# Kernel tuning notes

Measured on AMD Instinct MI355X. Metric: run time of the kernel, lower is better.

## Reference

```python
import jax, jax.numpy as jnp
import numpy as np

BIG = 1e11  # torch code replaces zero counts with 1e11 before dividing
N_LABELS = 5


def _label_mean(state, func):
    """Masked mean per label (1..5). state [..., S, H], func [..., S] int.
    Returns aug [..., 5, H], aug_mask [..., 5] bool. Zero-count labels -> 0
    (sum is exactly 0 and denom is BIG, matching the torch zero-init path)."""
    mask = (func[..., None] == jnp.arange(1, N_LABELS + 1)).astype(state.dtype)  # [...,S,5]
    sums = jnp.einsum('...sl,...sh->...lh', mask, state)                          # [...,5,H]
    counts = mask.sum(axis=-2)                                                    # [...,5]
    aug_mask = counts > 0
    denom = jnp.where(aug_mask, counts, jnp.asarray(BIG, state.dtype))
    return sums / denom[..., None], aug_mask


def _masked_mean(state, func):
    """Mean over all non-pad (func != 0) sentences. state [..., S, H]."""
    m = (func != 0).astype(state.dtype)
    s = jnp.einsum('...s,...sh->...h', m, state)
    c = m.sum(axis=-1)
    pm = c > 0
    denom = jnp.where(pm, c, jnp.asarray(BIG, state.dtype))
    return s / denom[..., None], pm


def setup_inputs() -> dict:
    key = jax.random.key(0)
    k1, k2, k3, k4 = jax.random.split(key, 4)
    B, TS, H = 8, 512, 512       # batch, tar_n_sents, enc_hidden_size
    D, RS = 32, 256              # ref_n_docs, ref_n_sents
    return {
        'tarsent_state': jax.random.normal(k1, (B, TS, H), jnp.float32),
        'tar_func': jax.random.randint(k2, (B, TS), 0, 6),
        'refsent_state': jax.random.normal(k3, (B, D, RS, H), jnp.float32),
        'ref_func': jax.random.randint(k4, (B, D, RS), 0, 6),
    }


def reference(tarsent_state, tar_func, refsent_state, ref_func):
    # tar_aug_state [B,5,H], tar_aug_mask [B,5]
    tar_aug, tar_aug_mask = _label_mean(tarsent_state, tar_func)
    # ref_aug_state [B,D,5,H], ref_aug_mask [B,D,5]
    ref_aug, ref_aug_mask = _label_mean(refsent_state, ref_func)
    # tarpaper_state [B,H], refpaper_state [B,D,H]
    tarpaper_state, tar_mask2 = _masked_mean(tarsent_state, tar_func)
    refpaper_state, ref_mask2 = _masked_mean(refsent_state, ref_func)
    return (tar_aug, tar_aug_mask, ref_aug, ref_aug_mask,
            tarpaper_state, tar_mask2, refpaper_state, ref_mask2)
```

## Files before the change

### kernel.cpp

```cpp
#include <hip/hip_runtime.h>


#define H      512
#define HV     128
#define NL     5
#define BIGF   1e11f
#define CHUNK  64
#define NITER  (CHUNK / 2)
#define BATCH  8

#define OFF_TAR_AUG       0
#define OFF_TAR_AUG_MASK  20480
#define OFF_REF_AUG       20520
#define OFF_REF_AUG_MASK  675880
#define OFF_TARPAPER      677160
#define OFF_TAR_MASK2     681256
#define OFF_REFPAPER      681264
#define OFF_REF_MASK2     812336

#define NCHUNK_REF 4
#define NCHUNK_TAR 8
#define NBLK_REF   1024
#define NBLK1      1088
#define WSUM_ELEMS ((size_t)NBLK1 * NL * H)
#define WCNT_OFF_B (WSUM_ELEMS * 4)
#define WS_NEED    (WCNT_OFF_B + (size_t)NBLK1 * NL * 4)

__device__ inline float4 f4add(float4 a, float4 b) {
    a.x += b.x; a.y += b.y; a.z += b.z; a.w += b.w; return a;
}
__device__ inline float4 f4scale(float4 a, float s) {
    a.x *= s; a.y *= s; a.z *= s; a.w *= s; return a;
}
__device__ inline float4 f4fma(float w, float4 v, float4 a) {
    a.x = fmaf(w, v.x, a.x); a.y = fmaf(w, v.y, a.y);
    a.z = fmaf(w, v.z, a.z); a.w = fmaf(w, v.w, a.w); return a;
}

__global__ __launch_bounds__(256) void emenc_stage1(
    const float* __restrict__ tar_state, const int* __restrict__ tar_func,
    const float* __restrict__ ref_state, const int* __restrict__ ref_func,
    float* __restrict__ wsum, int* __restrict__ wcnt)
{
    __shared__ int    sfunc[CHUNK];
    __shared__ float4 spart[HV * NL];

    const int b = blockIdx.x;
    const float* state;
    const int*   func;
    int s0;
    if (b < NBLK_REF) {
        const int seg = b >> 2, ch = b & 3;
        state = ref_state + (size_t)seg * 256 * H;
        func  = ref_func  + seg * 256;
        s0    = ch * CHUNK;
    } else {
        const int q = b - NBLK_REF;
        const int seg = q >> 3, ch = q & 7;
        state = tar_state + (size_t)seg * 512 * H;
        func  = tar_func  + seg * 512;
        s0    = ch * CHUNK;
    }

    const int tid = threadIdx.x;
    if (tid < CHUNK) sfunc[tid] = func[s0 + tid];
    __syncthreads();

    const int col   = tid & (HV - 1);
    const int phase = tid >> 7;

    float4 a1 = {0,0,0,0}, a2 = {0,0,0,0}, a3 = {0,0,0,0},
           a4 = {0,0,0,0}, a5 = {0,0,0,0};

    const float4* colp = ((const float4*)(state + (size_t)s0 * H)) + col
                         + (size_t)phase * HV;

    #pragma unroll
    for (int batch = 0; batch < NITER / BATCH; ++batch) {
        const int j0 = batch * BATCH;
        float4 v[BATCH];
        int    lb[BATCH];
        #pragma unroll
        for (int k = 0; k < BATCH; ++k)
            v[k] = colp[(size_t)(2 * (j0 + k)) * HV];
        #pragma unroll
        for (int k = 0; k < BATCH; ++k)
            lb[k] = sfunc[2 * (j0 + k) + phase];
        #pragma unroll
        for (int k = 0; k < BATCH; ++k) {
            const int l = lb[k];
            const float w1 = (l == 1) ? 1.0f : 0.0f;
            const float w2 = (l == 2) ? 1.0f : 0.0f;
            const float w3 = (l == 3) ? 1.0f : 0.0f;
            const float w4 = (l == 4) ? 1.0f : 0.0f;
            const float w5 = (l == 5) ? 1.0f : 0.0f;
            a1 = f4fma(w1, v[k], a1);
            a2 = f4fma(w2, v[k], a2);
            a3 = f4fma(w3, v[k], a3);
            a4 = f4fma(w4, v[k], a4);
            a5 = f4fma(w5, v[k], a5);
        }
    }

    if (phase == 1) {
        spart[col * NL + 0] = a1;
        spart[col * NL + 1] = a2;
        spart[col * NL + 2] = a3;
        spart[col * NL + 3] = a4;
        spart[col * NL + 4] = a5;
    }
    __syncthreads();

    if (phase == 0) {
        a1 = f4add(a1, spart[col * NL + 0]);
        a2 = f4add(a2, spart[col * NL + 1]);
        a3 = f4add(a3, spart[col * NL + 2]);
        a4 = f4add(a4, spart[col * NL + 3]);
        a5 = f4add(a5, spart[col * NL + 4]);

        float* wb = wsum + (size_t)b * NL * H;
        ((float4*)(wb + 0 * H))[col] = a1;
        ((float4*)(wb + 1 * H))[col] = a2;
        ((float4*)(wb + 2 * H))[col] = a3;
        ((float4*)(wb + 3 * H))[col] = a4;
        ((float4*)(wb + 4 * H))[col] = a5;
    }

    if (tid < NL) {
        int c = 0;
        #pragma unroll
        for (int i = 0; i < CHUNK; ++i) c += (sfunc[i] == tid + 1) ? 1 : 0;
        wcnt[b * NL + tid] = c;
    }
}

__global__ __launch_bounds__(128) void emenc_stage2(
    const float* __restrict__ wsum, const int* __restrict__ wcnt,
    float* __restrict__ out)
{
    const int bb   = blockIdx.x;
    const int seg  = bb / 6;
    const int role = bb - seg * 6;

    int nch, wb0;
    float *aug, *augmask, *paper, *mask2;
    if (seg < 256) {
        nch = NCHUNK_REF; wb0 = seg * NCHUNK_REF;
        aug     = out + OFF_REF_AUG      + (size_t)seg * NL * H;
        augmask = out + OFF_REF_AUG_MASK + seg * NL;
        paper   = out + OFF_REFPAPER     + (size_t)seg * H;
        mask2   = out + OFF_REF_MASK2    + seg;
    } else {
        const int q = seg - 256;
        nch = NCHUNK_TAR; wb0 = NBLK_REF + q * NCHUNK_TAR;
        aug     = out + OFF_TAR_AUG      + (size_t)q * NL * H;
        augmask = out + OFF_TAR_AUG_MASK + q * NL;
        paper   = out + OFF_TARPAPER     + (size_t)q * H;
        mask2   = out + OFF_TAR_MASK2    + q;
    }

    const int col = threadIdx.x;

    if (role < NL) {
        int c = 0;
        for (int ch = 0; ch < nch; ch++) c += wcnt[(wb0 + ch) * NL + role];
        float4 s = {0,0,0,0};
        for (int ch = 0; ch < nch; ch++)
            s = f4add(s, ((const float4*)(wsum + (size_t)(wb0 + ch) * NL * H
                                          + (size_t)role * H))[col]);
        const float inv = 1.0f / (c > 0 ? (float)c : BIGF);
        ((float4*)(aug + (size_t)role * H))[col] = f4scale(s, inv);
        if (col == 0) augmask[role] = c > 0 ? 1.0f : 0.0f;
    } else {
        int ct = 0;
        for (int ch = 0; ch < nch; ch++) {
            #pragma unroll
            for (int l = 0; l < NL; l++) ct += wcnt[(wb0 + ch) * NL + l];
        }
        float4 t = {0,0,0,0};
        for (int ch = 0; ch < nch; ch++) {
            const float4* wb = (const float4*)(wsum + (size_t)(wb0 + ch) * NL * H);
            #pragma unroll
            for (int l = 0; l < NL; l++) t = f4add(t, wb[l * HV + col]);
        }
        ((float4*)paper)[col] = f4scale(t, 1.0f / (ct > 0 ? (float)ct : BIGF));
        if (col == 0) mask2[0] = ct > 0 ? 1.0f : 0.0f;
    }
}

__global__ __launch_bounds__(256) void emenc_single(
    const float* __restrict__ tar_state, const int* __restrict__ tar_func,
    const float* __restrict__ ref_state, const int* __restrict__ ref_func,
    float* __restrict__ out)
{
    __shared__ int    sfunc[512];
    __shared__ float4 spart[HV * NL];
    __shared__ int    scnt[NL];

    const int b = blockIdx.x;
    const float* state;
    const int*   func;
    int S;
    float *aug, *augmask, *paper, *mask2;

    if (b < 256) {
        state   = ref_state + (size_t)b * 256 * H;
        func    = ref_func  + b * 256;
        S       = 256;
        aug     = out + OFF_REF_AUG      + (size_t)b * NL * H;
        augmask = out + OFF_REF_AUG_MASK + b * NL;
        paper   = out + OFF_REFPAPER     + (size_t)b * H;
        mask2   = out + OFF_REF_MASK2    + b;
    } else {
        const int q = b - 256;
        state   = tar_state + (size_t)q * 512 * H;
        func    = tar_func  + q * 512;
        S       = 512;
        aug     = out + OFF_TAR_AUG      + (size_t)q * NL * H;
        augmask = out + OFF_TAR_AUG_MASK + q * NL;
        paper   = out + OFF_TARPAPER     + (size_t)q * H;
        mask2   = out + OFF_TAR_MASK2    + q;
    }

    const int tid = threadIdx.x;
    for (int i = tid; i < S; i += 256) sfunc[i] = func[i];
    __syncthreads();

    const int col   = tid & (HV - 1);
    const int phase = tid >> 7;

    float4 a1 = {0,0,0,0}, a2 = {0,0,0,0}, a3 = {0,0,0,0},
           a4 = {0,0,0,0}, a5 = {0,0,0,0};

    for (int s = phase; s < S; s += 2) {
        float4 v = ((const float4*)(state + (size_t)s * H))[col];
        const int l = sfunc[s];
        a1 = f4fma((l == 1) ? 1.0f : 0.0f, v, a1);
        a2 = f4fma((l == 2) ? 1.0f : 0.0f, v, a2);
        a3 = f4fma((l == 3) ? 1.0f : 0.0f, v, a3);
        a4 = f4fma((l == 4) ? 1.0f : 0.0f, v, a4);
        a5 = f4fma((l == 5) ? 1.0f : 0.0f, v, a5);
    }

    if (phase == 1) {
        spart[col * NL + 0] = a1;
        spart[col * NL + 1] = a2;
        spart[col * NL + 2] = a3;
        spart[col * NL + 3] = a4;
        spart[col * NL + 4] = a5;
    }
    if (tid < NL) {
        int c = 0;
        for (int i = 0; i < S; ++i) c += (sfunc[i] == tid + 1) ? 1 : 0;
        scnt[tid] = c;
    }
    __syncthreads();

    if (phase == 0) {
        a1 = f4add(a1, spart[col * NL + 0]);
        a2 = f4add(a2, spart[col * NL + 1]);
        a3 = f4add(a3, spart[col * NL + 2]);
        a4 = f4add(a4, spart[col * NL + 3]);
        a5 = f4add(a5, spart[col * NL + 4]);

        const int c1 = scnt[0], c2 = scnt[1], c3 = scnt[2],
                  c4 = scnt[3], c5 = scnt[4];
        float4 t  = f4add(f4add(f4add(a1, a2), f4add(a3, a4)), a5);
        const int ct = c1 + c2 + c3 + c4 + c5;

        ((float4*)(aug + 0 * H))[col] = f4scale(a1, 1.0f / (c1 > 0 ? (float)c1 : BIGF));
        ((float4*)(aug + 1 * H))[col] = f4scale(a2, 1.0f / (c2 > 0 ? (float)c2 : BIGF));
        ((float4*)(aug + 2 * H))[col] = f4scale(a3, 1.0f / (c3 > 0 ? (float)c3 : BIGF));
        ((float4*)(aug + 3 * H))[col] = f4scale(a4, 1.0f / (c4 > 0 ? (float)c4 : BIGF));
        ((float4*)(aug + 4 * H))[col] = f4scale(a5, 1.0f / (c5 > 0 ? (float)c5 : BIGF));
        ((float4*)paper)[col]         = f4scale(t,  1.0f / (ct > 0 ? (float)ct : BIGF));

        if (col == 0) {
            augmask[0] = c1 > 0 ? 1.0f : 0.0f;
            augmask[1] = c2 > 0 ? 1.0f : 0.0f;
            augmask[2] = c3 > 0 ? 1.0f : 0.0f;
            augmask[3] = c4 > 0 ? 1.0f : 0.0f;
            augmask[4] = c5 > 0 ? 1.0f : 0.0f;
            mask2[0]   = ct > 0 ? 1.0f : 0.0f;
        }
    }
}

extern "C" void kernel_launch(void* const* d_in, const int* in_sizes, int n_in,
                              void* d_out, int out_size, void* d_ws, size_t ws_size,
                              hipStream_t stream) {
    const float* tar_state = (const float*)d_in[0];
    const int*   tar_func  = (const int*)d_in[1];
    const float* ref_state = (const float*)d_in[2];
    const int*   ref_func  = (const int*)d_in[3];
    float* out = (float*)d_out;

    if (ws_size >= WS_NEED) {
        float* wsum = (float*)d_ws;
        int*   wcnt = (int*)((char*)d_ws + WCNT_OFF_B);
        emenc_stage1<<<NBLK1, 256, 0, stream>>>(tar_state, tar_func,
                                                ref_state, ref_func, wsum, wcnt);
        emenc_stage2<<<264 * 6, 128, 0, stream>>>(wsum, wcnt, out);
    } else {
        emenc_single<<<264, 256, 0, stream>>>(tar_state, tar_func,
                                              ref_state, ref_func, out);
    }
}
```

Measured before the change: 210.7 us.

## Compact non-pad rows and stream them into LDS via async global_load_lds

Stage 1 now compacts each 64-row chunk down to the rows whose label is nonzero, using wave ballots, and computes the per-label counts with popcount. Only those rows are loaded, 8 at a time, through global_load_lds async copies into shared memory, then accumulated from LDS. This skips reading pad rows (about a sixth of the input) but adds LDS staging, two barriers per 8-row chunk and a serial load-then-compute loop with no double buffering. That may lose memory-level parallelism compared with the earlier batched register loads.

```diff
diff --git a/kernel.cpp b/kernel.cpp
--- a/kernel.cpp
+++ b/kernel.cpp
@@ -6,8 +6,7 @@
 #define NL     5
 #define BIGF   1e11f
 #define CHUNK  64
-#define NITER  (CHUNK / 2)
-#define BATCH  8
+#define RPC    8
 
 #define OFF_TAR_AUG       0
 #define OFF_TAR_AUG_MASK  20480
@@ -36,14 +35,23 @@
     a.x = fmaf(w, v.x, a.x); a.y = fmaf(w, v.y, a.y);
     a.z = fmaf(w, v.z, a.z); a.w = fmaf(w, v.w, a.w); return a;
 }
+__device__ inline void async_copy16(const float* g, float* l) {
+    __builtin_amdgcn_global_load_lds(
+        (const __attribute__((address_space(1))) void*)g,
+        (__attribute__((address_space(3))) void*)l, 16, 0, 0);
+}
 
 __global__ __launch_bounds__(256) void emenc_stage1(
     const float* __restrict__ tar_state, const int* __restrict__ tar_func,
     const float* __restrict__ ref_state, const int* __restrict__ ref_func,
     float* __restrict__ wsum, int* __restrict__ wcnt)
 {
-    __shared__ int    sfunc[CHUNK];
+    __shared__ float  sbuf[RPC * H];
     __shared__ float4 spart[HV * NL];
+    __shared__ int    crow[CHUNK];
+    __shared__ int    clab[CHUNK];
+    __shared__ int    scnt5[NL];
+    __shared__ int    sm;
 
     const int b = blockIdx.x;
     const float* state;
@@ -63,43 +71,65 @@
     }
 
     const int tid = threadIdx.x;
-    if (tid < CHUNK) sfunc[tid] = func[s0 + tid];
+
+    if (tid < CHUNK) {
+        const int l = func[s0 + tid];
+        #pragma unroll
+        for (int q = 1; q <= NL; ++q) {
+            const unsigned long long mq = __ballot(l == q);
+            if (tid == 0) scnt5[q - 1] = (int)__popcll(mq);
+        }
+        const unsigned long long mask = __ballot(l != 0);
+        if (l != 0) {
+            const int pos = (int)__popcll(mask & ((1ull << tid) - 1ull));
+            crow[pos] = tid;
+            clab[pos] = l;
+        }
+        if (tid == 0) sm = (int)__popcll(mask);
+    }
     __syncthreads();
 
+    const int m     = sm;
     const int col   = tid & (HV - 1);
     const int phase = tid >> 7;
+    const int lane  = tid & 63;
+    const int wv    = tid >> 6;
 
     float4 a1 = {0,0,0,0}, a2 = {0,0,0,0}, a3 = {0,0,0,0},
            a4 = {0,0,0,0}, a5 = {0,0,0,0};
 
-    const float4* colp = ((const float4*)(state + (size_t)s0 * H)) + col
-                         + (size_t)phase * HV;
-
-    #pragma unroll
-    for (int batch = 0; batch < NITER / BATCH; ++batch) {
-        const int j0 = batch * BATCH;
-        float4 v[BATCH];
-        int    lb[BATCH];
+    const int nch = (m + RPC - 1) / RPC;
+    for (int c = 0; c < nch; ++c) {
+        const int r0   = c * RPC;
+        const int rem  = m - r0;
+        const int rows = rem < RPC ? rem : RPC;
+
         #pragma unroll
-        for (int k = 0; k < BATCH; ++k)
-            v[k] = colp[(size_t)(2 * (j0 + k)) * HV];
-        #pragma unroll
-        for (int k = 0; k < BATCH; ++k)
-            lb[k] = sfunc[2 * (j0 + k) + phase];
-        #pragma unroll
-        for (int k = 0; k < BATCH; ++k) {
-            const int l = lb[k];
-            const float w1 = (l == 1) ? 1.0f : 0.0f;
-            const float w2 = (l == 2) ? 1.0f : 0.0f;
-            const float w3 = (l == 3) ? 1.0f : 0.0f;
-            const float w4 = (l == 4) ? 1.0f : 0.0f;
-            const float w5 = (l == 5) ? 1.0f : 0.0f;
-            a1 = f4fma(w1, v[k], a1);
-            a2 = f4fma(w2, v[k], a2);
-            a3 = f4fma(w3, v[k], a3);
-            a4 = f4fma(w4, v[k], a4);
-            a5 = f4fma(w5, v[k], a5);
-        }
+        for (int k = 0; k < 4; ++k) {
+            const int j  = wv * 4 + k;
+            const int rs = j >> 1;
+            if (rs < rows) {
+                const int half = j & 1;
+                const int row  = crow[r0 + rs];
+                const float* g = state + (size_t)(s0 + row) * H
+                                 + half * 256 + lane * 4;
+                float* l = sbuf + rs * H + half * 256;
+                async_copy16(g, l);
+            }
+        }
+        __builtin_amdgcn_s_waitcnt(0xF70);
+        __syncthreads();
+
+        for (int r = phase; r < rows; r += 2) {
+            const int l = clab[r0 + r];
+            const float4 v = *(const float4*)(sbuf + r * H + col * 4);
+            a1 = f4fma((l == 1) ? 1.0f : 0.0f, v, a1);
+            a2 = f4fma((l == 2) ? 1.0f : 0.0f, v, a2);
+            a3 = f4fma((l == 3) ? 1.0f : 0.0f, v, a3);
+            a4 = f4fma((l == 4) ? 1.0f : 0.0f, v, a4);
+            a5 = f4fma((l == 5) ? 1.0f : 0.0f, v, a5);
+        }
+        __syncthreads();
     }
 
     if (phase == 1) {
@@ -125,13 +155,7 @@
         ((float4*)(wb + 3 * H))[col] = a4;
         ((float4*)(wb + 4 * H))[col] = a5;
     }
-
-    if (tid < NL) {
-        int c = 0;
-        #pragma unroll
-        for (int i = 0; i < CHUNK; ++i) c += (sfunc[i] == tid + 1) ? 1 : 0;
-        wcnt[b * NL + tid] = c;
-    }
+    if (tid < NL) wcnt[b * NL + tid] = scnt5[tid];
 }
 
 __global__ __launch_bounds__(128) void emenc_stage2(
```

Result: no change. 207.8 us (-1.4%).
